# Kernel optimization log

Measured on AMD Instinct MI355X. Metric: run time of the kernel, lower is better.

The kernel has to match this reference:

```python
import jax, jax.numpy as jnp
import numpy as np

N_NODES = 50000
N_EDGES = 800000
N_GRAPHS = 64
IN_DIM = 128
HID = 256
N_LAYERS = 4
N_PROT = 5
N_CLASSES = 1
EPS = 1e-12


def setup_inputs() -> dict:
    key = jax.random.key(0)
    ks = jax.random.split(key, 10)
    h = jax.random.normal(ks[0], (N_NODES, IN_DIM), jnp.float32)
    src = jax.random.randint(ks[1], (N_EDGES,), 0, N_NODES, dtype=jnp.int32)
    dst = jax.random.randint(ks[2], (N_EDGES,), 0, N_NODES, dtype=jnp.int32)
    graph_id = jnp.sort(jax.random.randint(ks[3], (N_NODES,), 0, N_GRAPHS, dtype=jnp.int32))
    W_emb = jax.random.normal(ks[4], (IN_DIM, HID), jnp.float32) * 0.05
    b_emb = jnp.zeros((HID,), jnp.float32)
    Ws = jax.random.normal(ks[5], (N_LAYERS, 2 * HID, HID), jnp.float32) * 0.05
    bs = jnp.zeros((N_LAYERS, HID), jnp.float32)
    p_pos = jax.random.uniform(ks[6], (N_PROT, HID), jnp.float32)
    p_neg = jax.random.uniform(ks[7], (N_PROT, HID), jnp.float32)
    W_fc = jax.random.normal(ks[8], (N_CLASSES, 2 * N_PROT), jnp.float32) * 0.1
    return dict(h=h, src=src, dst=dst, graph_id=graph_id, W_emb=W_emb,
                b_emb=b_emb, Ws=Ws, bs=bs, p_pos=p_pos, p_neg=p_neg, W_fc=W_fc)


def _segment_mean(x, seg, num):
    # sum over segments, divide by count (empty segments -> 0, like DGL mean)
    s = jax.ops.segment_sum(x, seg, num_segments=num)
    cnt = jax.ops.segment_sum(jnp.ones((x.shape[0],), x.dtype), seg, num_segments=num)
    return s / jnp.maximum(cnt, 1.0)[:, None]


def _forward(h, src, dst, graph_id, W_emb, b_emb, Ws, bs, p_pos, p_neg, W_fc):
    x = h @ W_emb + b_emb  # [N, HID]
    for l in range(N_LAYERS):
        # mean aggregation of neighbor messages (copy_src -> mean at dst)
        c = _segment_mean(x[src], dst, N_NODES)  # [N, HID]
        bundle = jnp.concatenate([x, c], axis=1) @ Ws[l] + bs[l]  # [N, HID]
        # F.normalize(p=2, dim=1) then relu activation, then residual add
        norm = jnp.linalg.norm(bundle, axis=1, keepdims=True)
        bundle = bundle / jnp.maximum(norm, EPS)
        x = x + jax.nn.relu(bundle)
    hg = _segment_mean(x, graph_id, N_GRAPHS)  # dgl.mean_nodes -> [G, HID]

    def sims(P):
        d = jnp.sum((hg[:, None, :] - P[None, :, :]) ** 2, axis=-1)  # [G, P]
        return jnp.log((d + 1.0) / (d + EPS))

    ss = jnp.concatenate([sims(p_pos), sims(p_neg)], axis=1)  # [G, 2P]
    y = ss @ W_fc.T  # [G, n_classes]
    return jax.nn.sigmoid(y).squeeze()


def reference(h, src, dst, graph_id, W_emb, b_emb, Ws, bs, p_pos, p_neg, W_fc):
    return _forward(h, src, dst, graph_id, W_emb, b_emb, Ws, bs, p_pos, p_neg, W_fc)
```

## Files before the change

### kernel.cpp

```cpp
#include <hip/hip_runtime.h>
#include <math.h>

#define N_NODESC 50000
#define NPAD 50048
#define N_EDGESC 800000
#define N_GRAPHSC 64
#define IN_DIMC 128
#define HIDC 256
#define N_LAYERSC 4
#define EPSV 1e-12f

#define NBUCK 196
#define EPB 4096
#define NBLK1 196
#define WCONV_BLKS 2176

typedef __attribute__((ext_vector_type(8))) short short8;
typedef __attribute__((ext_vector_type(4))) float floatx4;
typedef __attribute__((ext_vector_type(2))) float floatx2;

__device__ __forceinline__ unsigned short f2b(float f) {
    union { float f; unsigned u; } v; v.f = f;
    unsigned r = v.u + 0x7FFFu + ((v.u >> 16) & 1u);
    return (unsigned short)(r >> 16);
}
__device__ __forceinline__ unsigned pkb(float a, float b) {
    return (unsigned)f2b(a) | ((unsigned)f2b(b) << 16);
}
__device__ __forceinline__ unsigned char f2q(float v) {
    return (unsigned char)(__builtin_amdgcn_cvt_pk_fp8_f32(v, v, 0, false) & 0xFF);
}
__device__ __forceinline__ float q2f(unsigned u) {
    floatx2 t = __builtin_amdgcn_cvt_pk_f32_fp8(u, false);
    return t.x;
}
__device__ __forceinline__ unsigned pk4q(float a, float b, float c, float d) {
    unsigned lo = (unsigned)__builtin_amdgcn_cvt_pk_fp8_f32(a, b, 0, false) & 0xFFFFu;
    unsigned hi = (unsigned)__builtin_amdgcn_cvt_pk_fp8_f32(c, d, 0, false) << 16;
    return lo | hi;
}
__device__ __forceinline__ void ldscp16(const void* g, void* l) {
    __builtin_amdgcn_global_load_lds(
        (const __attribute__((address_space(1))) unsigned int*)g,
        (__attribute__((address_space(3))) unsigned int*)l, 16, 0, 0);
}
__device__ __forceinline__ void acc8(uint2 v, float* a) {
    floatx2 t0 = __builtin_amdgcn_cvt_pk_f32_fp8(v.x, false);
    floatx2 t1 = __builtin_amdgcn_cvt_pk_f32_fp8(v.x, true);
    floatx2 t2 = __builtin_amdgcn_cvt_pk_f32_fp8(v.y, false);
    floatx2 t3 = __builtin_amdgcn_cvt_pk_f32_fp8(v.y, true);
    a[0] += t0.x; a[1] += t0.y; a[2] += t1.x; a[3] += t1.y;
    a[4] += t2.x; a[5] += t2.y; a[6] += t3.x; a[7] += t3.y;
}

__global__ __launch_bounds__(256) void k_pre1(const float* __restrict__ Wemb,
        const float* __restrict__ Ws, unsigned short* __restrict__ wsw,
        unsigned char* __restrict__ wq, const int* __restrict__ gid,
        int* __restrict__ gstart, const int* __restrict__ dst,
        int* __restrict__ gbcnt) {
    __shared__ int bc[256];
    int b = blockIdx.x;
    int t = threadIdx.x;
    if (b < WCONV_BLKS) {
        int idx = b * 256 + t;
        const int EMB = IN_DIMC * HIDC;
        const int LYR = 2 * HIDC * HIDC;
        if (idx < EMB) {
            int k = idx >> 8, n = idx & 255;
            int off = (((k >> 5) * 16 + (n >> 4)) * 64 + ((((k >> 3) & 3) << 4) | (n & 15))) * 8 + (k & 7);
            wsw[off] = f2b(Wemb[idx]);
        } else if (idx < EMB + N_LAYERSC * LYR) {
            int r = idx - EMB;
            int l = r >> 17;
            int r2 = r & (LYR - 1);
            int k = r2 >> 8, n = r2 & 255;
            int off = (((k >> 5) * 16 + (n >> 4)) * 64 + ((((k >> 3) & 3) << 4) | (n & 15))) * 8 + (k & 7);
            wq[(size_t)l * LYR + off] = f2q(Ws[r]);
        }
    } else if (b == WCONV_BLKS) {
        int g = t;
        if (g <= N_GRAPHSC) {
            int lo = 0, hi = N_NODESC;
            while (lo < hi) {
                int mid = (lo + hi) >> 1;
                if (gid[mid] < g) lo = mid + 1; else hi = mid;
            }
            gstart[g] = lo;
        }
    } else {
        bc[t] = 0;
        __syncthreads();
        int e0 = (b - WCONV_BLKS - 1) * EPB;
        for (int i = t; i < EPB; i += 256) {
            int e = e0 + i;
            if (e < N_EDGESC) atomicAdd(&bc[dst[e] >> 8], 1);
        }
        __syncthreads();
        if (t < NBUCK && bc[t] > 0) atomicAdd(&gbcnt[t], bc[t]);
    }
}

__global__ __launch_bounds__(256) void k_bscan(const int* __restrict__ gbcnt,
        int* __restrict__ boffB, int* __restrict__ gcurB) {
    __shared__ int s[256];
    int t = threadIdx.x;
    int v = (t < NBUCK) ? gbcnt[t] : 0;
    s[t] = v;
    __syncthreads();
    for (int d = 1; d < 256; d <<= 1) {
        int u = (t >= d) ? s[t - d] : 0;
        __syncthreads();
        s[t] += u;
        __syncthreads();
    }
    if (t < NBUCK) {
        int excl = s[t] - v;
        boffB[t] = excl;
        gcurB[t] = excl;
    }
    if (t == 0) boffB[NBUCK] = N_EDGESC;
}

__global__ __launch_bounds__(256, 4) void k_scat_egemm(const int* __restrict__ src,
        const int* __restrict__ dst, int* __restrict__ gcurB,
        unsigned* __restrict__ ebpack, const float* __restrict__ h,
        const unsigned short* __restrict__ wsw, const float* __restrict__ bias,
        unsigned char* __restrict__ xq) {
    __shared__ int bc[256];
    __shared__ int cur[256];
    if (blockIdx.x < NBLK1) {
        int t = threadIdx.x;
        bc[t] = 0;
        __syncthreads();
        int e0 = blockIdx.x * EPB;
        for (int i = t; i < EPB; i += 256) {
            int e = e0 + i;
            if (e < N_EDGESC) atomicAdd(&bc[dst[e] >> 8], 1);
        }
        __syncthreads();
        if (t < NBUCK)
            cur[t] = (bc[t] > 0) ? atomicAdd(&gcurB[t], bc[t]) : 0;
        __syncthreads();
        for (int i = t; i < EPB; i += 256) {
            int e = e0 + i;
            if (e < N_EDGESC) {
                int d = dst[e];
                int b = d >> 8;
                int pos = atomicAdd(&cur[b], 1);
                ebpack[pos] = (unsigned)src[e] | ((unsigned)(d & 255) << 16);
            }
        }
        return;
    }
    int tid = threadIdx.x;
    int wn = tid >> 6;
    int lane = tid & 63;
    int quad = lane >> 4;
    int l15 = lane & 15;
    int row0 = (blockIdx.x - NBLK1) * 32;

    floatx4 acc[2][4];
    #pragma unroll
    for (int mt = 0; mt < 2; mt++)
        #pragma unroll
        for (int n = 0; n < 4; n++)
            acc[mt][n] = (floatx4){0.f, 0.f, 0.f, 0.f};

    int r0 = row0 + l15;
    int r1 = row0 + 16 + l15;
    bool ok0 = r0 < N_NODESC, ok1 = r1 < N_NODESC;
    const float* h0 = h + (size_t)r0 * IN_DIMC + quad * 8;
    const float* h1 = h + (size_t)r1 * IN_DIMC + quad * 8;
    const unsigned short* bp = wsw + ((size_t)(wn * 4) * 64 + lane) * 8;

    #pragma unroll
    for (int ks = 0; ks < 4; ks++) {
        float4 f00 = ok0 ? *(const float4*)(h0 + ks * 32)     : (float4){0,0,0,0};
        float4 f01 = ok0 ? *(const float4*)(h0 + ks * 32 + 4) : (float4){0,0,0,0};
        float4 f10 = ok1 ? *(const float4*)(h1 + ks * 32)     : (float4){0,0,0,0};
        float4 f11 = ok1 ? *(const float4*)(h1 + ks * 32 + 4) : (float4){0,0,0,0};
        short8 afr[2], bfr[4];
        uint4 av;
        av.x = pkb(f00.x, f00.y); av.y = pkb(f00.z, f00.w);
        av.z = pkb(f01.x, f01.y); av.w = pkb(f01.z, f01.w);
        afr[0] = *(short8*)&av;
        av.x = pkb(f10.x, f10.y); av.y = pkb(f10.z, f10.w);
        av.z = pkb(f11.x, f11.y); av.w = pkb(f11.z, f11.w);
        afr[1] = *(short8*)&av;
        const unsigned short* wp = bp + (size_t)ks * 8192;
        #pragma unroll
        for (int n = 0; n < 4; n++)
            bfr[n] = *(const short8*)(wp + n * 512);
        #pragma unroll
        for (int mt = 0; mt < 2; mt++)
            #pragma unroll
            for (int n = 0; n < 4; n++)
                acc[mt][n] = __builtin_amdgcn_mfma_f32_16x16x32_bf16(
                    afr[mt], bfr[n], acc[mt][n], 0, 0, 0);
    }

    float bv[4];
    #pragma unroll
    for (int n = 0; n < 4; n++) bv[n] = bias[wn * 64 + n * 16 + l15];
    #pragma unroll
    for (int mt = 0; mt < 2; mt++) {
        #pragma unroll
        for (int r = 0; r < 4; r++) {
            int row = row0 + mt * 16 + quad * 4 + r;
            if (row < N_NODESC) {
                #pragma unroll
                for (int n = 0; n < 4; n++) {
                    int col = wn * 64 + n * 16 + l15;
                    float v = acc[mt][n][r] + bv[n];
                    xq[(size_t)row * HIDC + col] = f2q(v);
                }
            }
        }
    }
}

__global__ __launch_bounds__(256) void k_bbuild(const unsigned* __restrict__ ebpack,
        const int* __restrict__ boffB, int* __restrict__ offs,
        unsigned short* __restrict__ esrc) {
    __shared__ int deg[256];
    __shared__ int lofs[256];
    __shared__ unsigned short img[12288];
    int b = blockIdx.x;
    int t = threadIdx.x;
    int bbase = boffB[b];
    int cnt = boffB[b + 1] - bbase;
    deg[t] = 0;
    __syncthreads();
    for (int i = t; i < cnt; i += 256)
        atomicAdd(&deg[ebpack[bbase + i] >> 16], 1);
    __syncthreads();
    int v = deg[t];
    lofs[t] = v;
    __syncthreads();
    for (int d = 1; d < 256; d <<= 1) {
        int u = (t >= d) ? lofs[t - d] : 0;
        __syncthreads();
        lofs[t] += u;
        __syncthreads();
    }
    int excl = lofs[t] - v;
    int node = b * 256 + t;
    if (node < N_NODESC) offs[node] = bbase + excl;
    if (b == NBUCK - 1 && t == 0) offs[N_NODESC] = N_EDGESC;
    deg[t] = excl;
    __syncthreads();
    for (int i = t; i < cnt; i += 256) {
        unsigned p = ebpack[bbase + i];
        int pos = atomicAdd(&deg[p >> 16], 1);
        img[pos] = (unsigned short)(p & 0xFFFF);
    }
    __syncthreads();
    for (int i = t; i < cnt; i += 256)
        esrc[bbase + i] = img[i];
}

template<bool LAST>
__global__ __launch_bounds__(256, 6) void k_layer(const unsigned char* __restrict__ xqin,
        unsigned char* __restrict__ xqout, const unsigned char* __restrict__ wq,
        const float* __restrict__ bias, const int* __restrict__ offs,
        const unsigned short* __restrict__ esrc, const int* __restrict__ gid,
        float* __restrict__ hg) {
    __shared__ unsigned long long panelA64[1024];
    __shared__ unsigned long long panelC64[1024];
    __shared__ float rs[32];
    __shared__ float hgp[LAST ? 1024 : 1];
    __shared__ signed char ggl[LAST ? 32 : 1];
    __shared__ int g0s;
    unsigned char* panelA = (unsigned char*)panelA64;
    unsigned char* panelC = (unsigned char*)panelC64;
    int tid = threadIdx.x;
    int w = tid >> 6;
    int lane = tid & 63;
    int quad = lane >> 4;
    int l15 = lane & 15;
    int row0 = blockIdx.x * 32;

    {
        int sboff = w * 2048 + lane * 16;
        #pragma unroll
        for (int i = 0; i < 2; i++) {
            int ldsoff = sboff + i * 1024;
            int r = ldsoff >> 8;
            int ch = (ldsoff & 255) >> 4;
            int lc = ch ^ (r & 15);
            ldscp16(xqin + (size_t)(row0 + r) * HIDC + lc * 16, &panelA[w * 2048 + i * 1024]);
        }
    }

    {
        int lane32 = tid & 31;
        int sub = tid >> 5;
        size_t loff = (size_t)lane32 * 8;
        #pragma unroll 1
        for (int grp = 0; grp < 4; grp++) {
            int lrow = grp * 8 + sub;
            int node = row0 + lrow;
            float a[8];
            #pragma unroll
            for (int j = 0; j < 8; j++) a[j] = 0.f;
            int beg = 0, end = 0;
            if (node < N_NODESC) { beg = offs[node]; end = offs[node + 1]; }
            int e = beg;
            for (; e + 8 <= end; e += 8) {
                int sidx[8];
                #pragma unroll
                for (int j = 0; j < 8; j++) sidx[j] = esrc[e + j];
                uint2 v[8];
                #pragma unroll
                for (int j = 0; j < 8; j++)
                    v[j] = *(const uint2*)(xqin + (size_t)sidx[j] * HIDC + loff);
                #pragma unroll
                for (int j = 0; j < 8; j++) acc8(v[j], a);
            }
            if (e + 4 <= end) {
                int sidx[4];
                #pragma unroll
                for (int j = 0; j < 4; j++) sidx[j] = esrc[e + j];
                uint2 v[4];
                #pragma unroll
                for (int j = 0; j < 4; j++)
                    v[j] = *(const uint2*)(xqin + (size_t)sidx[j] * HIDC + loff);
                #pragma unroll
                for (int j = 0; j < 4; j++) acc8(v[j], a);
                e += 4;
            }
            for (; e < end; e++) {
                uint2 v = *(const uint2*)(xqin + (size_t)esrc[e] * HIDC + loff);
                acc8(v, a);
            }
            float wm = 1.0f / (float)max(end - beg, 1);
            uint2 o;
            o.x = pk4q(a[0] * wm, a[1] * wm, a[2] * wm, a[3] * wm);
            o.y = pk4q(a[4] * wm, a[5] * wm, a[6] * wm, a[7] * wm);
            int phys = (lane32 >> 1) ^ (lrow & 15);
            *(uint2*)&panelC[lrow * 256 + phys * 16 + (lane32 & 1) * 8] = o;
        }
    }
    __syncthreads();

    floatx4 acc[2][4];
    #pragma unroll
    for (int mt = 0; mt < 2; mt++)
        #pragma unroll
        for (int n = 0; n < 4; n++)
            acc[mt][n] = (floatx4){0.f, 0.f, 0.f, 0.f};

    const unsigned char* bp = wq + ((size_t)(w * 4) * 64 + lane) * 8;

    #pragma unroll
    for (int st = 0; st < 16; st++) {
        const unsigned char* pan = (st < 8) ? panelA : panelC;
        int ks = st & 7;
        long long afr[2], bfr[4];
        #pragma unroll
        for (int mt = 0; mt < 2; mt++) {
            int row = mt * 16 + l15;
            int lc = ks * 2 + (quad >> 1);
            int phys = lc ^ (row & 15);
            afr[mt] = *(const long long*)&pan[row * 256 + phys * 16 + (quad & 1) * 8];
        }
        const unsigned char* wp = bp + (size_t)st * 8192;
        #pragma unroll
        for (int n = 0; n < 4; n++)
            bfr[n] = *(const long long*)(wp + n * 512);
        #pragma unroll
        for (int mt = 0; mt < 2; mt++)
            #pragma unroll
            for (int n = 0; n < 4; n++)
                acc[mt][n] = __builtin_amdgcn_mfma_f32_16x16x32_fp8_fp8(
                    afr[mt], bfr[n], acc[mt][n], 0, 0, 0);
    }

    float bv[4];
    #pragma unroll
    for (int n = 0; n < 4; n++) bv[n] = bias[w * 64 + n * 16 + l15];
    #pragma unroll
    for (int mt = 0; mt < 2; mt++)
        #pragma unroll
        for (int n = 0; n < 4; n++)
            #pragma unroll
            for (int r = 0; r < 4; r++)
                acc[mt][n][r] += bv[n];

    __syncthreads();
    if (tid < 32) rs[tid] = 0.f;
    if constexpr (LAST) {
        #pragma unroll
        for (int i = 0; i < 4; i++) hgp[i * 256 + tid] = 0.f;
        if (tid < 32) {
            int g0 = gid[min(row0, N_NODESC - 1)];
            int gv = gid[min(row0 + tid, N_NODESC - 1)] - g0;
            ggl[tid] = (signed char)min(gv, 3);
            if (tid == 0) g0s = g0;
        }
    }
    __syncthreads();
    #pragma unroll
    for (int mt = 0; mt < 2; mt++) {
        #pragma unroll
        for (int r = 0; r < 4; r++) {
            float p = acc[mt][0][r] * acc[mt][0][r] + acc[mt][1][r] * acc[mt][1][r]
                    + acc[mt][2][r] * acc[mt][2][r] + acc[mt][3][r] * acc[mt][3][r];
            p += __shfl_xor(p, 1);
            p += __shfl_xor(p, 2);
            p += __shfl_xor(p, 4);
            p += __shfl_xor(p, 8);
            if (l15 == 0) atomicAdd(&rs[mt * 16 + quad * 4 + r], p);
        }
    }
    __syncthreads();

    #pragma unroll
    for (int mt = 0; mt < 2; mt++) {
        #pragma unroll
        for (int r = 0; r < 4; r++) {
            int lrow = mt * 16 + quad * 4 + r;
            int row = row0 + lrow;
            if (row < N_NODESC) {
                float inv = 1.0f / fmaxf(sqrtf(rs[mt * 16 + quad * 4 + r]), EPSV);
                #pragma unroll
                for (int n = 0; n < 4; n++) {
                    int col = w * 64 + n * 16 + l15;
                    int phys = (w * 4 + n) ^ (lrow & 15);
                    float xo = q2f((unsigned)panelA[lrow * 256 + phys * 16 + l15]);
                    float nv = xo + fmaxf(acc[mt][n][r] * inv, 0.f);
                    if constexpr (LAST) {
                        atomicAdd(&hgp[(int)ggl[lrow] * 256 + col], nv);
                    } else {
                        xqout[(size_t)row * HIDC + col] = f2q(nv);
                    }
                }
            }
        }
    }
    if constexpr (LAST) {
        __syncthreads();
        if (row0 < N_NODESC) {
            int nspan = (int)ggl[31] + 1;
            int g0 = g0s;
            for (int gl = 0; gl < nspan; gl++)
                atomicAdd(&hg[(g0 + gl) * HIDC + tid], hgp[gl * 256 + tid]);
        }
    }
}

__global__ __launch_bounds__(256) void k_readout(const float* __restrict__ hg,
        const int* __restrict__ gstart, const float* __restrict__ ppos,
        const float* __restrict__ pneg, const float* __restrict__ wfc,
        float* __restrict__ out) {
    __shared__ float red[256];
    __shared__ float ss[10];
    int t = threadIdx.x;
    int g = blockIdx.x;
    int beg = gstart[g], end = gstart[g + 1];
    float inv = 1.0f / (float)max(end - beg, 1);
    float hgv = hg[g * HIDC + t] * inv;
    for (int p = 0; p < 10; p++) {
        const float* P = (p < 5) ? (ppos + p * HIDC) : (pneg + (p - 5) * HIDC);
        float d = hgv - P[t];
        red[t] = d * d;
        __syncthreads();
        for (int s2 = 128; s2 > 0; s2 >>= 1) {
            if (t < s2) red[t] += red[t + s2];
            __syncthreads();
        }
        if (t == 0) {
            float dd = red[0];
            ss[p] = logf((dd + 1.0f) / (dd + EPSV));
        }
        __syncthreads();
    }
    if (t == 0) {
        float y = 0.f;
        #pragma unroll
        for (int p = 0; p < 10; p++) y += ss[p] * wfc[p];
        out[g] = 1.0f / (1.0f + expf(-y));
    }
}

extern "C" void kernel_launch(void* const* d_in, const int* in_sizes, int n_in,
                              void* d_out, int out_size, void* d_ws, size_t ws_size,
                              hipStream_t stream) {
    const float* h    = (const float*)d_in[0];
    const int*   src  = (const int*)d_in[1];
    const int*   dst  = (const int*)d_in[2];
    const int*   gid  = (const int*)d_in[3];
    const float* Wemb = (const float*)d_in[4];
    const float* bemb = (const float*)d_in[5];
    const float* Ws   = (const float*)d_in[6];
    const float* bs   = (const float*)d_in[7];
    const float* ppos = (const float*)d_in[8];
    const float* pneg = (const float*)d_in[9];
    const float* wfc  = (const float*)d_in[10];
    float* out = (float*)d_out;

    char* ws = (char*)d_ws;
    size_t off = 0;
    auto alloc = [&](size_t bytes) {
        void* p = ws + off;
        off += (bytes + 255) & ~(size_t)255;
        return p;
    };
    unsigned char*  xqA    = (unsigned char*)alloc((size_t)NPAD * HIDC);
    unsigned char*  xqB    = (unsigned char*)alloc((size_t)NPAD * HIDC);
    unsigned short* wsw    = (unsigned short*)alloc((size_t)(IN_DIMC * HIDC) * 2);
    unsigned char*  wq     = (unsigned char*)alloc((size_t)(N_LAYERSC * 2 * HIDC * HIDC));
    int*            offs   = (int*)alloc((size_t)(N_NODESC + 1) * 4);
    unsigned short* esrc   = (unsigned short*)alloc((size_t)N_EDGESC * 2);
    unsigned*       ebpack = (unsigned*)alloc((size_t)N_EDGESC * 4);
    int*            gbcnt  = (int*)alloc((size_t)NBUCK * 4);
    int*            boffB  = (int*)alloc((size_t)(NBUCK + 1) * 4);
    int*            gcurB  = (int*)alloc((size_t)NBUCK * 4);
    int*            gstart = (int*)alloc((size_t)(N_GRAPHSC + 1) * 4);
    float*          hg     = (float*)alloc((size_t)N_GRAPHSC * HIDC * 4);
    (void)ws_size; (void)in_sizes; (void)n_in; (void)out_size;

    hipMemsetAsync(gbcnt, 0, (size_t)NBUCK * 4, stream);
    hipMemsetAsync(hg, 0, (size_t)N_GRAPHSC * HIDC * 4, stream);

    const int LYR = 2 * HIDC * HIDC;
    k_pre1<<<WCONV_BLKS + 1 + NBLK1, 256, 0, stream>>>(Wemb, Ws, wsw, wq, gid, gstart, dst, gbcnt);
    k_bscan<<<1, 256, 0, stream>>>(gbcnt, boffB, gcurB);
    k_scat_egemm<<<NBLK1 + NPAD / 32, 256, 0, stream>>>(src, dst, gcurB, ebpack, h, wsw, bemb, xqA);
    k_bbuild<<<NBUCK, 256, 0, stream>>>(ebpack, boffB, offs, esrc);

    k_layer<false><<<NPAD / 32, 256, 0, stream>>>(xqA, xqB, wq + (size_t)0 * LYR, bs + 0 * HIDC, offs, esrc, gid, hg);
    k_layer<false><<<NPAD / 32, 256, 0, stream>>>(xqB, xqA, wq + (size_t)1 * LYR, bs + 1 * HIDC, offs, esrc, gid, hg);
    k_layer<false><<<NPAD / 32, 256, 0, stream>>>(xqA, xqB, wq + (size_t)2 * LYR, bs + 2 * HIDC, offs, esrc, gid, hg);
    k_layer<true ><<<NPAD / 32, 256, 0, stream>>>(xqB, xqA, wq + (size_t)3 * LYR, bs + 3 * HIDC, offs, esrc, gid, hg);

    k_readout<<<N_GRAPHSC, 256, 0, stream>>>(hg, gstart, ppos, pneg, wfc, out);
}
```

Measured before the change: 407.1 us.

## Split neighbor aggregation out of fused layer kernel into separate kernel

Each layer's fused aggregate+GEMM kernel becomes two kernels. A standalone aggregation kernel assigns 32 lanes per node and writes the fp8 mean to a global buffer. The GEMM kernel then loads both x and aggregate panels through async global-to-LDS copies and updates x in place. This is meant to let the irregular gather run at higher occupancy, separate from the register- and LDS-heavy GEMM. In exchange it adds an extra launch and a write and read of the aggregate buffer per layer.

Result: slower. 433.2 us (+6.4%).

```diff
diff --git a/kernel.cpp b/kernel.cpp
--- a/kernel.cpp
+++ b/kernel.cpp
@@ -43,14 +43,6 @@
     __builtin_amdgcn_global_load_lds(
         (const __attribute__((address_space(1))) unsigned int*)g,
         (__attribute__((address_space(3))) unsigned int*)l, 16, 0, 0);
-}
-__device__ __forceinline__ void acc8(uint2 v, float* a) {
-    floatx2 t0 = __builtin_amdgcn_cvt_pk_f32_fp8(v.x, false);
-    floatx2 t1 = __builtin_amdgcn_cvt_pk_f32_fp8(v.x, true);
-    floatx2 t2 = __builtin_amdgcn_cvt_pk_f32_fp8(v.y, false);
-    floatx2 t3 = __builtin_amdgcn_cvt_pk_f32_fp8(v.y, true);
-    a[0] += t0.x; a[1] += t0.y; a[2] += t1.x; a[3] += t1.y;
-    a[4] += t2.x; a[5] += t2.y; a[6] += t3.x; a[7] += t3.y;
 }
 
 __global__ __launch_bounds__(256) void k_pre1(const float* __restrict__ Wemb,
@@ -259,11 +251,66 @@
         esrc[bbase + i] = img[i];
 }
 
+__global__ __launch_bounds__(256, 8) void k_aggregate(const unsigned char* __restrict__ xq,
+        const int* __restrict__ offs, const unsigned short* __restrict__ esrc,
+        unsigned char* __restrict__ cq) {
+    int gidx = blockIdx.x * 256 + threadIdx.x;
+    int node = gidx >> 5;
+    int lane = threadIdx.x & 31;
+    if (node >= N_NODESC) return;
+    int beg = offs[node], end = offs[node + 1];
+    float a[8];
+    #pragma unroll
+    for (int j = 0; j < 8; j++) a[j] = 0.f;
+    size_t loff = (size_t)lane * 8;
+    int e = beg;
+    #define ACC8(v) do { \
+        floatx2 t0 = __builtin_amdgcn_cvt_pk_f32_fp8((v).x, false); \
+        floatx2 t1 = __builtin_amdgcn_cvt_pk_f32_fp8((v).x, true);  \
+        floatx2 t2 = __builtin_amdgcn_cvt_pk_f32_fp8((v).y, false); \
+        floatx2 t3 = __builtin_amdgcn_cvt_pk_f32_fp8((v).y, true);  \
+        a[0] += t0.x; a[1] += t0.y; a[2] += t1.x; a[3] += t1.y;     \
+        a[4] += t2.x; a[5] += t2.y; a[6] += t3.x; a[7] += t3.y;     \
+    } while (0)
+    for (; e + 8 <= end; e += 8) {
+        int sidx[8];
+        #pragma unroll
+        for (int j = 0; j < 8; j++) sidx[j] = esrc[e + j];
+        uint2 v[8];
+        #pragma unroll
+        for (int j = 0; j < 8; j++)
+            v[j] = *(const uint2*)(xq + (size_t)sidx[j] * HIDC + loff);
+        #pragma unroll
+        for (int j = 0; j < 8; j++) ACC8(v[j]);
+    }
+    if (e + 4 <= end) {
+        int sidx[4];
+        #pragma unroll
+        for (int j = 0; j < 4; j++) sidx[j] = esrc[e + j];
+        uint2 v[4];
+        #pragma unroll
+        for (int j = 0; j < 4; j++)
+            v[j] = *(const uint2*)(xq + (size_t)sidx[j] * HIDC + loff);
+        #pragma unroll
+        for (int j = 0; j < 4; j++) ACC8(v[j]);
+        e += 4;
+    }
+    for (; e < end; e++) {
+        uint2 v = *(const uint2*)(xq + (size_t)esrc[e] * HIDC + loff);
+        ACC8(v);
+    }
+    #undef ACC8
+    float w = 1.0f / (float)max(end - beg, 1);
+    uint2 o;
+    o.x = pk4q(a[0] * w, a[1] * w, a[2] * w, a[3] * w);
+    o.y = pk4q(a[4] * w, a[5] * w, a[6] * w, a[7] * w);
+    *(uint2*)(cq + (size_t)node * HIDC + loff) = o;
+}
+
 template<bool LAST>
-__global__ __launch_bounds__(256, 6) void k_layer(const unsigned char* __restrict__ xqin,
-        unsigned char* __restrict__ xqout, const unsigned char* __restrict__ wq,
-        const float* __restrict__ bias, const int* __restrict__ offs,
-        const unsigned short* __restrict__ esrc, const int* __restrict__ gid,
+__global__ __launch_bounds__(256, 6) void k_lgemm(unsigned char* __restrict__ xq,
+        const unsigned char* __restrict__ cq, const unsigned char* __restrict__ wq,
+        const float* __restrict__ bias, const int* __restrict__ gid,
         float* __restrict__ hg) {
     __shared__ unsigned long long panelA64[1024];
     __shared__ unsigned long long panelC64[1024];
@@ -288,57 +335,8 @@
             int r = ldsoff >> 8;
             int ch = (ldsoff & 255) >> 4;
             int lc = ch ^ (r & 15);
-            ldscp16(xqin + (size_t)(row0 + r) * HIDC + lc * 16, &panelA[w * 2048 + i * 1024]);
-        }
-    }
-
-    {
-        int lane32 = tid & 31;
-        int sub = tid >> 5;
-        size_t loff = (size_t)lane32 * 8;
-        #pragma unroll 1
-        for (int grp = 0; grp < 4; grp++) {
-            int lrow = grp * 8 + sub;
-            int node = row0 + lrow;
-            float a[8];
-            #pragma unroll
-            for (int j = 0; j < 8; j++) a[j] = 0.f;
-            int beg = 0, end = 0;
-            if (node < N_NODESC) { beg = offs[node]; end = offs[node + 1]; }
-            int e = beg;
-            for (; e + 8 <= end; e += 8) {
-                int sidx[8];
-                #pragma unroll
-                for (int j = 0; j < 8; j++) sidx[j] = esrc[e + j];
-                uint2 v[8];
-                #pragma unroll
-                for (int j = 0; j < 8; j++)
-                    v[j] = *(const uint2*)(xqin + (size_t)sidx[j] * HIDC + loff);
-                #pragma unroll
-                for (int j = 0; j < 8; j++) acc8(v[j], a);
-            }
-            if (e + 4 <= end) {
-                int sidx[4];
-                #pragma unroll
-                for (int j = 0; j < 4; j++) sidx[j] = esrc[e + j];
-                uint2 v[4];
-                #pragma unroll
-                for (int j = 0; j < 4; j++)
-                    v[j] = *(const uint2*)(xqin + (size_t)sidx[j] * HIDC + loff);
-                #pragma unroll
-                for (int j = 0; j < 4; j++) acc8(v[j], a);
-                e += 4;
-            }
-            for (; e < end; e++) {
-                uint2 v = *(const uint2*)(xqin + (size_t)esrc[e] * HIDC + loff);
-                acc8(v, a);
-            }
-            float wm = 1.0f / (float)max(end - beg, 1);
-            uint2 o;
-            o.x = pk4q(a[0] * wm, a[1] * wm, a[2] * wm, a[3] * wm);
-            o.y = pk4q(a[4] * wm, a[5] * wm, a[6] * wm, a[7] * wm);
-            int phys = (lane32 >> 1) ^ (lrow & 15);
-            *(uint2*)&panelC[lrow * 256 + phys * 16 + (lane32 & 1) * 8] = o;
+            ldscp16(xq + (size_t)(row0 + r) * HIDC + lc * 16, &panelA[w * 2048 + i * 1024]);
+            ldscp16(cq + (size_t)(row0 + r) * HIDC + lc * 16, &panelC[w * 2048 + i * 1024]);
         }
     }
     __syncthreads();
@@ -432,7 +430,7 @@
                     if constexpr (LAST) {
                         atomicAdd(&hgp[(int)ggl[lrow] * 256 + col], nv);
                     } else {
-                        xqout[(size_t)row * HIDC + col] = f2q(nv);
+                        xq[(size_t)row * HIDC + col] = f2q(nv);
                     }
                 }
             }
@@ -506,8 +504,8 @@
         off += (bytes + 255) & ~(size_t)255;
         return p;
     };
-    unsigned char*  xqA    = (unsigned char*)alloc((size_t)NPAD * HIDC);
-    unsigned char*  xqB    = (unsigned char*)alloc((size_t)NPAD * HIDC);
+    unsigned char*  xq     = (unsigned char*)alloc((size_t)NPAD * HIDC);
+    unsigned char*  cq     = (unsigned char*)alloc((size_t)NPAD * HIDC);
     unsigned short* wsw    = (unsigned short*)alloc((size_t)(IN_DIMC * HIDC) * 2);
     unsigned char*  wq     = (unsigned char*)alloc((size_t)(N_LAYERSC * 2 * HIDC * HIDC));
     int*            offs   = (int*)alloc((size_t)(N_NODESC + 1) * 4);
@@ -526,13 +524,17 @@
     const int LYR = 2 * HIDC * HIDC;
     k_pre1<<<WCONV_BLKS + 1 + NBLK1, 256, 0, stream>>>(Wemb, Ws, wsw, wq, gid, gstart, dst, gbcnt);
     k_bscan<<<1, 256, 0, stream>>>(gbcnt, boffB, gcurB);
-    k_scat_egemm<<<NBLK1 + NPAD / 32, 256, 0, stream>>>(src, dst, gcurB, ebpack, h, wsw, bemb, xqA);
+    k_scat_egemm<<<NBLK1 + NPAD / 32, 256, 0, stream>>>(src, dst, gcurB, ebpack, h, wsw, bemb, xq);
     k_bbuild<<<NBUCK, 256, 0, stream>>>(ebpack, boffB, offs, esrc);
 
-    k_layer<false><<<NPAD / 32, 256, 0, stream>>>(xqA, xqB, wq + (size_t)0 * LYR, bs + 0 * HIDC, offs, esrc, gid, hg);
-    k_layer<false><<<NPAD / 32, 256, 0, stream>>>(xqB, xqA, wq + (size_t)1 * LYR, bs + 1 * HIDC, offs, esrc, gid, hg);
-    k_layer<false><<<NPAD / 32, 256, 0, stream>>>(xqA, xqB, wq + (size_t)2 * LYR, bs + 2 * HIDC, offs, esrc, gid, hg);
-    k_layer<true ><<<NPAD / 32, 256, 0, stream>>>(xqB, xqA, wq + (size_t)3 * LYR, bs + 3 * HIDC, offs, esrc, gid, hg);
-
+    for (int l = 0; l < N_LAYERSC; l++) {
+        k_aggregate<<<(N_NODESC * 32 + 255) / 256, 256, 0, stream>>>(xq, offs, esrc, cq);
+        if (l < N_LAYERSC - 1)
+            k_lgemm<false><<<NPAD / 32, 256, 0, stream>>>(
+                xq, cq, wq + (size_t)l * LYR, bs + (size_t)l * HIDC, gid, hg);
+        else
+            k_lgemm<true><<<NPAD / 32, 256, 0, stream>>>(
+                xq, cq, wq + (size_t)l * LYR, bs + (size_t)l * HIDC, gid, hg);
+    }
     k_readout<<<N_GRAPHSC, 256, 0, stream>>>(hg, gstart, ppos, pneg, wfc, out);
 }
```
